# Kernel optimization log

Hardware: AMD Instinct MI355X
Metric: run time of the kernel (lower is better)

Reference implementation:

```python
import jax, jax.numpy as jnp
import numpy as np

NUM_EXPERTS = 16
NUM_K = 2


def setup_inputs() -> dict:
    key = jax.random.key(0)
    k1, k2 = jax.random.split(key)
    x = jax.random.normal(k1, (8, 8192, 1024), dtype=jnp.float32)
    W = jax.random.normal(k2, (NUM_EXPERTS, 1024), dtype=jnp.float32) * (1.0 / np.sqrt(1024))
    b = jnp.zeros((NUM_EXPERTS,), dtype=jnp.float32)
    return {"x": x, "W": W, "b": b}


def reference(x, W, b):
    # logits: [B, S, E]
    logits = jnp.einsum('bsd,ed->bse', x, W) + b
    weights = jax.nn.softmax(logits, axis=-1)
    # top-k over experts, then scatter values back into a sparse gate mask
    topk_vals, topk_idx = jax.lax.top_k(weights, NUM_K)  # [B, S, k]
    # one-hot scatter (E is small, so [B,S,k,E] intermediate is cheap)
    gated = (jax.nn.one_hot(topk_idx, NUM_EXPERTS, dtype=weights.dtype)
             * topk_vals[..., None]).sum(axis=-2)  # [B, S, E]
    # permute(2, 0, 1): [E, B, S]
    return gated.transpose(2, 0, 1), weights.transpose(2, 0, 1)
```

## Files before the change

### kernel.cpp

```cpp
#include <hip/hip_runtime.h>
#include <math.h>


constexpr int D     = 1024;
constexpr int NE    = 16;
constexpr int NTOK  = 8 * 8192;
constexpr int TPB   = 256;
constexpr int TOKS  = 64;
constexpr int PARTS = 4;
constexpr int PDIM  = D / PARTS;
constexpr int CF4   = 8;
constexpr int NCH   = PDIM / (CF4 * 4);
constexpr int LSTR  = NE * PARTS + 4;

__global__ __launch_bounds__(TPB, 4) void gating_kernel(
    const float* __restrict__ x,
    const float* __restrict__ W,
    const float* __restrict__ bias,
    float* __restrict__ out)
{
    __shared__ float lds[TOKS * LSTR];
    const int t    = threadIdx.x;
    const int lane = t & 63;
    const int wv   = t >> 6;
    const long tok = (long)blockIdx.x * TOKS + lane;

    const float4* __restrict__ xr4 = (const float4*)(x + tok * D + (long)wv * PDIM);
    const float4* __restrict__ Wp4 = (const float4*)(W + wv * PDIM);

    float acc[NE];
    #pragma unroll
    for (int e = 0; e < NE; ++e) acc[e] = 0.0f;

    #pragma unroll 1
    for (int c = 0; c < NCH; ++c) {
        float4 pf[CF4];
        #pragma unroll
        for (int j = 0; j < CF4; ++j) pf[j] = xr4[c * CF4 + j];

        #pragma unroll
        for (int e = 0; e < NE; ++e) {
            #pragma unroll
            for (int j = 0; j < CF4; ++j) {
                const float4 w4 = Wp4[e * (D / 4) + c * CF4 + j];
                acc[e] = fmaf(pf[j].x, w4.x, acc[e]);
                acc[e] = fmaf(pf[j].y, w4.y, acc[e]);
                acc[e] = fmaf(pf[j].z, w4.z, acc[e]);
                acc[e] = fmaf(pf[j].w, w4.w, acc[e]);
            }
        }
    }

    #pragma unroll
    for (int e = 0; e < NE; ++e)
        lds[lane * LSTR + e * 4 + wv] = acc[e];
    __syncthreads();

    float logits[NE];
    float m = -INFINITY;
    #pragma unroll
    for (int e = 0; e < NE; ++e) {
        const float4 p = *(const float4*)&lds[lane * LSTR + e * 4];
        logits[e] = p.x + p.y + p.z + p.w + bias[e];
        m = fmaxf(m, logits[e]);
    }
    float w[NE];
    float s = 0.0f;
    #pragma unroll
    for (int e = 0; e < NE; ++e) {
        w[e] = __expf(logits[e] - m);
        s += w[e];
    }
    const float inv = 1.0f / s;
    #pragma unroll
    for (int e = 0; e < NE; ++e) w[e] *= inv;

    float b1 = -1.0f; int i1 = 0;
    float b2 = -1.0f; int i2 = 0;
    #pragma unroll
    for (int e = 0; e < NE; ++e) {
        if (w[e] > b1)      { b2 = b1; i2 = i1; b1 = w[e]; i1 = e; }
        else if (w[e] > b2) { b2 = w[e]; i2 = e; }
    }

    float* __restrict__ out0 = out;
    float* __restrict__ out1 = out + (long)NE * NTOK;
    #pragma unroll
    for (int i = 0; i < NE / PARTS; ++i) {
        const int e = wv * (NE / PARTS) + i;
        const float g = (e == i1) ? b1 : ((e == i2) ? b2 : 0.0f);
        out0[(long)e * NTOK + tok] = g;
        out1[(long)e * NTOK + tok] = w[e];
    }
}

extern "C" void kernel_launch(void* const* d_in, const int* in_sizes, int n_in,
                              void* d_out, int out_size, void* d_ws, size_t ws_size,
                              hipStream_t stream) {
    const float* x = (const float*)d_in[0];
    const float* W = (const float*)d_in[1];
    const float* b = (const float*)d_in[2];
    float* out = (float*)d_out;

    dim3 grid(NTOK / TOKS);
    dim3 block(TPB);
    gating_kernel<<<grid, block, 0, stream>>>(x, W, b, out);
}
```

Before: 453.4 us.

## Stage x tiles in double-buffered LDS with coalesced loads, split experts across waves

Replaces per-lane strided row reads of x (each lane reading its own token's row) with cooperative coalesced float4 loads into a double-buffered, padded LDS tile. Loads for the next chunk are prefetched into registers while the current chunk is computed. Each wave now computes 4 experts over the full D instead of all 16 experts over a quarter of D, and W addresses are made wave-uniform via readfirstlane so they can be fetched as scalar loads. This adds a __syncthreads per chunk and extra LDS traffic in exchange for better global-memory coalescing.

```diff
diff --git a/kernel.cpp b/kernel.cpp
--- a/kernel.cpp
+++ b/kernel.cpp
@@ -2,16 +2,17 @@
 #include <math.h>
 
 
-constexpr int D     = 1024;
-constexpr int NE    = 16;
-constexpr int NTOK  = 8 * 8192;
-constexpr int TPB   = 256;
-constexpr int TOKS  = 64;
-constexpr int PARTS = 4;
-constexpr int PDIM  = D / PARTS;
-constexpr int CF4   = 8;
-constexpr int NCH   = PDIM / (CF4 * 4);
-constexpr int LSTR  = NE * PARTS + 4;
+constexpr int D    = 1024;
+constexpr int D4   = D / 4;
+constexpr int NE   = 16;
+constexpr int NTOK = 8 * 8192;
+constexpr int TPB  = 256;
+constexpr int TOKS = 64;
+constexpr int CH4  = 16;
+constexpr int NCH  = D4 / CH4;
+constexpr int TSTR = CH4 + 1;
+constexpr int EPW  = NE / 4;
+constexpr int LSTR = NE + 4;
 
 __global__ __launch_bounds__(TPB, 4) void gating_kernel(
     const float* __restrict__ x,
@@ -19,49 +20,65 @@
     const float* __restrict__ bias,
     float* __restrict__ out)
 {
-    __shared__ float lds[TOKS * LSTR];
-    const int t    = threadIdx.x;
-    const int lane = t & 63;
-    const int wv   = t >> 6;
-    const long tok = (long)blockIdx.x * TOKS + lane;
+    __shared__ float4 tile[2][TOKS * TSTR];
+    const int tid  = threadIdx.x;
+    const int lane = tid & 63;
+    const int wv   = tid >> 6;
+    const long blockTok = (long)blockIdx.x * TOKS;
 
-    const float4* __restrict__ xr4 = (const float4*)(x + tok * D + (long)wv * PDIM);
-    const float4* __restrict__ Wp4 = (const float4*)(W + wv * PDIM);
+    const int srow = tid >> 4;
+    const int scol = tid & 15;
+    const float4* __restrict__ xg = (const float4*)x + blockTok * D4;
 
-    float acc[NE];
+    const float4* __restrict__ Wq =
+        (const float4*)W + (size_t)__builtin_amdgcn_readfirstlane(wv * EPW * D4);
+
+    float4 pf[4];
     #pragma unroll
-    for (int e = 0; e < NE; ++e) acc[e] = 0.0f;
+    for (int s = 0; s < 4; ++s)
+        pf[s] = xg[(s * 16 + srow) * D4 + scol];
+
+    float acc[EPW];
+    #pragma unroll
+    for (int i = 0; i < EPW; ++i) acc[i] = 0.0f;
 
     #pragma unroll 1
     for (int c = 0; c < NCH; ++c) {
-        float4 pf[CF4];
         #pragma unroll
-        for (int j = 0; j < CF4; ++j) pf[j] = xr4[c * CF4 + j];
-
+        for (int s = 0; s < 4; ++s)
+            tile[c & 1][(s * 16 + srow) * TSTR + scol] = pf[s];
+        __syncthreads();
+        if (c + 1 < NCH) {
+            #pragma unroll
+            for (int s = 0; s < 4; ++s)
+                pf[s] = xg[(s * 16 + srow) * D4 + (c + 1) * CH4 + scol];
+        }
+        const float4* __restrict__ row = &tile[c & 1][lane * TSTR];
         #pragma unroll
-        for (int e = 0; e < NE; ++e) {
+        for (int j = 0; j < CH4; ++j) {
+            const float4 xv = row[j];
             #pragma unroll
-            for (int j = 0; j < CF4; ++j) {
-                const float4 w4 = Wp4[e * (D / 4) + c * CF4 + j];
-                acc[e] = fmaf(pf[j].x, w4.x, acc[e]);
-                acc[e] = fmaf(pf[j].y, w4.y, acc[e]);
-                acc[e] = fmaf(pf[j].z, w4.z, acc[e]);
-                acc[e] = fmaf(pf[j].w, w4.w, acc[e]);
+            for (int i = 0; i < EPW; ++i) {
+                const float4 w4 = Wq[i * D4 + c * CH4 + j];
+                acc[i] = fmaf(xv.x, w4.x, acc[i]);
+                acc[i] = fmaf(xv.y, w4.y, acc[i]);
+                acc[i] = fmaf(xv.z, w4.z, acc[i]);
+                acc[i] = fmaf(xv.w, w4.w, acc[i]);
             }
         }
     }
 
+    float* lbuf = (float*)&tile[0][0];
     #pragma unroll
-    for (int e = 0; e < NE; ++e)
-        lds[lane * LSTR + e * 4 + wv] = acc[e];
+    for (int i = 0; i < EPW; ++i)
+        lbuf[lane * LSTR + wv * EPW + i] = acc[i];
     __syncthreads();
 
     float logits[NE];
     float m = -INFINITY;
     #pragma unroll
     for (int e = 0; e < NE; ++e) {
-        const float4 p = *(const float4*)&lds[lane * LSTR + e * 4];
-        logits[e] = p.x + p.y + p.z + p.w + bias[e];
+        logits[e] = lbuf[lane * LSTR + e] + bias[e];
         m = fmaxf(m, logits[e]);
     }
     float w[NE];
@@ -86,11 +103,11 @@
     float* __restrict__ out0 = out;
     float* __restrict__ out1 = out + (long)NE * NTOK;
     #pragma unroll
-    for (int i = 0; i < NE / PARTS; ++i) {
-        const int e = wv * (NE / PARTS) + i;
+    for (int i = 0; i < EPW; ++i) {
+        const int e = wv * EPW + i;
         const float g = (e == i1) ? b1 : ((e == i2) ? b2 : 0.0f);
-        out0[(long)e * NTOK + tok] = g;
-        out1[(long)e * NTOK + tok] = w[e];
+        out0[(long)e * NTOK + blockTok + lane] = g;
+        out1[(long)e * NTOK + blockTok + lane] = w[e];
     }
 }
 
```

After: 427.9 us. -5.6%, faster.
